# Kernel optimization log

Hardware: AMD Instinct MI355X
Metric: run time of the kernel (lower is better)

The kernel has to match this reference:

```python
import jax, jax.numpy as jnp
import numpy as np


def _scattering(image, mags, phases):
    # image: [B,S,S] real; mags/phases: [J,L,S,S] real (Fourier-domain Morlet filters)
    J = mags.shape[0]
    psi = (mags * jnp.exp(1j * phases)).astype(jnp.complex64)        # [J,L,S,S]
    xf = jnp.fft.fft2(image)                                          # [B,S,S] complex64
    # first-order: modulus of wavelet convolutions, all scales/orientations at once
    u1 = jnp.abs(jnp.fft.ifft2(xf[:, None, None] * psi[None]))        # [B,J,L,S,S]
    s0 = image.mean(axis=(-2, -1))                                    # [B]
    s1 = u1.mean(axis=(2, 3, 4))                                      # [B,J] (orientation-averaged)
    # second-order: only j2 > j1 (the nan-filtered entries in the original)
    s2_parts = []
    for j1 in range(J - 1):  # structural loop over scales, not data dims
        u1f = jnp.fft.fft2(u1[:, j1].astype(jnp.complex64))           # [B,L1,S,S]
        psi2 = psi[j1 + 1:]                                           # [J2,L2,S,S]
        v = jnp.abs(jnp.fft.ifft2(u1f[:, :, None, None] * psi2[None, None]))  # [B,L1,J2,L2,S,S]
        s2_parts.append(v.mean(axis=(1, 3, 4, 5)))                    # [B,J2]
    s2 = jnp.concatenate(s2_parts, axis=1)                            # [B, J*(J-1)/2]
    return s0, s1, s2


def setup_inputs() -> dict:
    key = jax.random.key(0)
    ks = jax.random.split(key, 8)
    B, S, J, L = 64, 128, 6, 4
    return {
        "image_batch": jax.random.normal(ks[0], (B, S, S), dtype=jnp.float32),
        "mags": jax.random.uniform(ks[1], (J, L, S, S), dtype=jnp.float32),
        "phases": jax.random.normal(ks[2], (J, L, S, S), dtype=jnp.float32),
        "w1": jax.random.normal(ks[3], (22, 16), dtype=jnp.float32) * 0.1,
        "b1": jnp.zeros((16,), dtype=jnp.float32),
        "w2": jax.random.normal(ks[4], (16, 16), dtype=jnp.float32) * 0.1,
        "b2": jnp.zeros((16,), dtype=jnp.float32),
        "w3": jax.random.normal(ks[5], (16, 1), dtype=jnp.float32) * 0.1,
        "b3": jnp.zeros((1,), dtype=jnp.float32),
    }


def reference(image_batch, mags, phases, w1, b1, w2, b2, w3, b3):
    s0, s1, s2 = _scattering(image_batch, mags, phases)
    x = jnp.concatenate([s0[:, None], s1, s2], axis=1)                # [B,22]
    x = jax.nn.relu(x @ w1 + b1)
    x = jax.nn.relu(x @ w2 + b2)
    x = jax.nn.sigmoid(x @ w3 + b3)
    return jnp.squeeze(x, axis=1)                                     # [B]
```

## Files before the change

kernel.cpp:

```cpp
#include <hip/hip_runtime.h>
#include <math.h>


#define SDIM 128
#define PLANE 16384
#define PITCH 129
#define NT 1024
#define TWO_PI 6.28318530717958647692f
#define PSIH_SCALE 16.0f
#define A_SCALE 16.0f

typedef _Float16 h2 __attribute__((ext_vector_type(2)));

constexpr float W16R[8] = {1.f, 0.9238795325f, 0.7071067812f, 0.3826834324f,
                           0.f, -0.3826834324f, -0.7071067812f, -0.9238795325f};
constexpr float W16I[8] = {0.f, -0.3826834324f, -0.7071067812f, -0.9238795325f,
                           -1.f, -0.9238795325f, -0.7071067812f, -0.3826834324f};

__device__ __forceinline__ float fast_sqrtf(float x) { return __builtin_amdgcn_sqrtf(x); }

__device__ __forceinline__ unsigned packbf(float re, float im) {
  const unsigned r = __float_as_uint(re) + 0x8000u;
  const unsigned i = __float_as_uint(im) + 0x8000u;
  return __builtin_amdgcn_perm(r, i, 0x07060302u);
}
__device__ __forceinline__ void unpackbf(unsigned u, float& re, float& im) {
  re = __uint_as_float(u & 0xFFFF0000u);
  im = __uint_as_float(u << 16);
}

union UHU { unsigned u; h2 h; };
__device__ __forceinline__ h2 u2h(unsigned u) { UHU x; x.u = u; return x.h; }
__device__ __forceinline__ unsigned h2u(h2 h) { UHU x; x.h = h; return x.u; }
__device__ __forceinline__ h2 bch2(float f) { const _Float16 h = (_Float16)f; h2 v = {h, h}; return v; }
__device__ __forceinline__ h2 mkh2(float a, float b) { h2 v = {(_Float16)a, (_Float16)b}; return v; }

#define SEL_LO 0x05040100u
#define SEL_HI 0x07060302u

__device__ __forceinline__ void stC(float2* s, int idx, float re, float im) { s[idx] = make_float2(re, im); }
__device__ __forceinline__ void ldC(const float2* s, int idx, float& re, float& im) { const float2 v = s[idx]; re = v.x; im = v.y; }
__device__ __forceinline__ void stC(unsigned* s, int idx, float re, float im) { s[idx] = packbf(re, im); }
__device__ __forceinline__ void ldC(const unsigned* s, int idx, float& re, float& im) { unpackbf(s[idx], re, im); }

__device__ __forceinline__ void load_tw(const float2* __restrict__ twg, int g,
                                        float* twr, float* twi) {
#pragma unroll
  for (int k = 1; k < 16; ++k) {
    const float2 w = twg[16 * g + k];
    twr[k] = __uint_as_float(__builtin_amdgcn_readfirstlane(__float_as_uint(w.x)));
    twi[k] = __uint_as_float(__builtin_amdgcn_readfirstlane(__float_as_uint(w.y)));
  }
}
__device__ __forceinline__ void load_twh(const uint2* __restrict__ twgh, int g,
                                         unsigned* twru, unsigned* twiu) {
#pragma unroll
  for (int k = 1; k < 16; ++k) {
    const uint2 w = twgh[16 * g + k];
    twru[k] = (unsigned)__builtin_amdgcn_readfirstlane((int)w.x);
    twiu[k] = (unsigned)__builtin_amdgcn_readfirstlane((int)w.y);
  }
}

template<bool INV>
__device__ __forceinline__ void bfly(float& ar, float& ai, float& br, float& bi, const int idx) {
  float tr, ti;
  if (idx == 0) { tr = br; ti = bi; }
  else if (idx == 4) {
    if (INV) { tr = -bi; ti = br; } else { tr = bi; ti = -br; }
  } else {
    const float wr = W16R[idx];
    const float wi = INV ? -W16I[idx] : W16I[idx];
    tr = br * wr - bi * wi;
    ti = br * wi + bi * wr;
  }
  br = ar - tr; bi = ai - ti;
  ar = ar + tr; ai = ai + ti;
}

#define CSWAP(re, im, a, b) { float _t = re[a]; re[a]=re[b]; re[b]=_t; _t = im[a]; im[a]=im[b]; im[b]=_t; }

template<bool INV>
__device__ __forceinline__ void dft16(float* re, float* im) {
  CSWAP(re, im, 1, 8) CSWAP(re, im, 2, 4) CSWAP(re, im, 3, 12)
  CSWAP(re, im, 5, 10) CSWAP(re, im, 7, 14) CSWAP(re, im, 11, 13)
#pragma unroll
  for (int ls = 1; ls <= 4; ++ls) {
    const int len = 1 << ls, half = len >> 1, tstep = 16 >> ls;
#pragma unroll
    for (int blk = 0; blk < 16; blk += len)
#pragma unroll
      for (int j = 0; j < half; ++j)
        bfly<INV>(re[blk + j], im[blk + j], re[blk + j + half], im[blk + j + half], j * tstep);
  }
}

template<bool INV>
__device__ __forceinline__ void dft8(float* re, float* im) {
  CSWAP(re, im, 1, 4) CSWAP(re, im, 3, 6)
#pragma unroll
  for (int ls = 1; ls <= 3; ++ls) {
    const int len = 1 << ls, half = len >> 1, tstep = 8 >> ls;
#pragma unroll
    for (int blk = 0; blk < 8; blk += len)
#pragma unroll
      for (int j = 0; j < half; ++j)
        bfly<INV>(re[blk + j], im[blk + j], re[blk + j + half], im[blk + j + half], j * tstep * 2);
  }
}

__device__ __forceinline__ void twmul_fwd(float* R, float* I, const float* twr, const float* twi) {
#pragma unroll
  for (int k = 1; k < 16; ++k) {
    const float r = R[k] * twr[k] - I[k] * twi[k];
    I[k] = R[k] * twi[k] + I[k] * twr[k]; R[k] = r;
  }
}
__device__ __forceinline__ void twmul_inv(float* R, float* I, const float* twr, const float* twi) {
#pragma unroll
  for (int k = 1; k < 16; ++k) {
    const float r = R[k] * twr[k] + I[k] * twi[k];
    I[k] = I[k] * twr[k] - R[k] * twi[k]; R[k] = r;
  }
}

template<typename S>
__device__ __forceinline__ void fwd_fft2(float* R, float* I, S* sC,
                                         int g, int q, const float* twr, const float* twi) {
  const int rb = q * PITCH;
  dft16<false>(R, I);
  twmul_fwd(R, I, twr, twi);
  __syncthreads();
#pragma unroll
  for (int k = 0; k < 16; ++k) stC(sC, rb + 8 * k + g, R[k], I[k]);
  __syncthreads();
#pragma unroll
  for (int t = 0; t < 8; ++t) {
    ldC(sC, rb + 16 * g + t, R[t], I[t]);
    ldC(sC, rb + 16 * g + 8 + t, R[8 + t], I[8 + t]);
  }
  dft8<false>(R, I); dft8<false>(R + 8, I + 8);
#pragma unroll
  for (int k2 = 0; k2 < 8; ++k2) {
    stC(sC, rb + 16 * g + k2, R[k2], I[k2]);
    stC(sC, rb + 16 * g + 8 + k2, R[8 + k2], I[8 + k2]);
  }
  __syncthreads();
#pragma unroll
  for (int m = 0; m < 16; ++m) ldC(sC, (g + 8 * m) * PITCH + q, R[m], I[m]);
  dft16<false>(R, I);
  twmul_fwd(R, I, twr, twi);
#pragma unroll
  for (int k = 0; k < 16; ++k) stC(sC, (8 * k + g) * PITCH + q, R[k], I[k]);
  __syncthreads();
#pragma unroll
  for (int u = 0; u < 8; ++u) {
    const int bp = (16 * g + 2 * u) * PITCH + q;
    ldC(sC, bp, R[2 * u], I[2 * u]);
    ldC(sC, bp + PITCH, R[2 * u + 1], I[2 * u + 1]);
  }
  dft8<false>(R, I); dft8<false>(R + 8, I + 8);
}

template<bool FIRST, typename S>
__device__ __forceinline__ void inv_fft2(float* R, float* I, S* sC,
                                         int g, int q, const float* twr, const float* twi) {
  const int rb = q * PITCH;
  dft8<true>(R, I); dft8<true>(R + 8, I + 8);
  if constexpr (!FIRST) __syncthreads();
#pragma unroll
  for (int t = 0; t < 16; ++t) stC(sC, rb + 16 * g + t, R[t], I[t]);
  __syncthreads();
#pragma unroll
  for (int k = 0; k < 16; ++k) ldC(sC, rb + 8 * k + g, R[k], I[k]);
  twmul_inv(R, I, twr, twi);
  dft16<true>(R, I);
#pragma unroll
  for (int m = 0; m < 16; ++m) stC(sC, rb + g + 8 * m, R[m], I[m]);
  __syncthreads();
#pragma unroll
  for (int u = 0; u < 8; ++u) {
    const int bp = (16 * g + 2 * u) * PITCH + q;
    ldC(sC, bp, R[2 * u], I[2 * u]);
    ldC(sC, bp + PITCH, R[2 * u + 1], I[2 * u + 1]);
  }
  dft8<true>(R, I); dft8<true>(R + 8, I + 8);
#pragma unroll
  for (int u = 0; u < 8; ++u) {
    const int bp = (16 * g + 2 * u) * PITCH + q;
    stC(sC, bp, R[2 * u], I[2 * u]);
    stC(sC, bp + PITCH, R[2 * u + 1], I[2 * u + 1]);
  }
  __syncthreads();
#pragma unroll
  for (int k = 0; k < 16; ++k) ldC(sC, (8 * k + g) * PITCH + q, R[k], I[k]);
  twmul_inv(R, I, twr, twi);
  dft16<true>(R, I);
}

template<bool INV>
__device__ __forceinline__ void bfly_h(h2& ar, h2& ai, h2& br, h2& bi, const int idx) {
  h2 tr, ti;
  if (idx == 0) { tr = br; ti = bi; }
  else if (idx == 4) {
    if (INV) { tr = -bi; ti = br; } else { tr = bi; ti = -br; }
  } else {
    const h2 wr = bch2(W16R[idx]);
    const h2 wi = bch2(INV ? -W16I[idx] : W16I[idx]);
    tr = br * wr - bi * wi;
// ... 64 lines not shown
#pragma unroll
  for (int k = 0; k < 16; ++k) { const uint2 v = sU[sb + 8 * k + g]; R2[k] = u2h(v.x); I2[k] = u2h(v.y); }
  twmul_inv_h(R2, I2, twru, twiu);
  dft16h<true>(R2, I2);
#pragma unroll
  for (int m = 0; m < 16; ++m) sU[sb + g + 8 * m] = make_uint2(h2u(R2[m]), h2u(I2[m]));
  __syncthreads();
  {
    const int s_base = (16 * g) & 63;
    const unsigned sel = (g < 4) ? SEL_LO : SEL_HI;
#pragma unroll
    for (int j = 0; j < 16; ++j) {
      const int cb = (s_base + j) * PITCH;
      const uint2 vA = sU[cb + q];
      const uint2 vB = sU[cb + q + 64];
      R2[j] = u2h(__builtin_amdgcn_perm(vB.x, vA.x, sel));
      I2[j] = u2h(__builtin_amdgcn_perm(vB.y, vA.y, sel));
    }
  }
  dft8h<true>(R2, I2); dft8h<true>(R2 + 8, I2 + 8);
  __syncthreads();
#pragma unroll
  for (int s = 0; s < 16; ++s) sU[sb + 16 * g + s] = make_uint2(h2u(R2[s]), h2u(I2[s]));
  __syncthreads();
#pragma unroll
  for (int k = 0; k < 16; ++k) { const uint2 v = sU[sb + 8 * k + g]; R2[k] = u2h(v.x); I2[k] = u2h(v.y); }
  twmul_inv_h(R2, I2, twru, twiu);
  dft16h<true>(R2, I2);
}

__device__ __forceinline__ void fwd_rp_core(h2* R2, h2* I2, uint2* sU,
                                            int g, int q,
                                            const unsigned* twru, const unsigned* twiu) {
  const int sb = q * PITCH;
  dft16h<false>(R2, I2);
  twmul_fwd_h(R2, I2, twru, twiu);
#pragma unroll
  for (int k = 0; k < 16; ++k) sU[sb + 8 * k + g] = make_uint2(h2u(R2[k]), h2u(I2[k]));
  __syncthreads();
#pragma unroll
  for (int t = 0; t < 16; ++t) { const uint2 v = sU[sb + 16 * g + t]; R2[t] = u2h(v.x); I2[t] = u2h(v.y); }
  dft8h<false>(R2, I2); dft8h<false>(R2 + 8, I2 + 8);
#pragma unroll
  for (int t = 0; t < 16; ++t) sU[sb + 16 * g + t] = make_uint2(h2u(R2[t]), h2u(I2[t]));
  __syncthreads();
  {
#pragma unroll
    for (int u = 0; u < 8; ++u) {
      const int cb = (g + 8 * u) * PITCH;
      const uint2 vA = sU[cb + q];
      const uint2 vB = sU[cb + q + 64];
      R2[u]     = u2h(__builtin_amdgcn_perm(vB.x, vA.x, SEL_LO));
      I2[u]     = u2h(__builtin_amdgcn_perm(vB.y, vA.y, SEL_LO));
      R2[u + 8] = u2h(__builtin_amdgcn_perm(vB.x, vA.x, SEL_HI));
      I2[u + 8] = u2h(__builtin_amdgcn_perm(vB.y, vA.y, SEL_HI));
    }
  }
  dft16h<false>(R2, I2);
  twmul_fwd_h(R2, I2, twru, twiu);
  __syncthreads();
#pragma unroll
  for (int k = 0; k < 16; ++k) sU[sb + 8 * k + g] = make_uint2(h2u(R2[k]), h2u(I2[k]));
  __syncthreads();
#pragma unroll
  for (int t = 0; t < 16; ++t) { const uint2 v = sU[sb + 16 * g + t]; R2[t] = u2h(v.x); I2[t] = u2h(v.y); }
  dft8h<false>(R2, I2); dft8h<false>(R2 + 8, I2 + 8);
}

template<int NW>
__device__ __forceinline__ float block_reduce_sum(float v, float* red, int tid) {
#pragma unroll
  for (int o = 32; o > 0; o >>= 1) v += __shfl_down(v, o);
  __syncthreads();
  if ((tid & 63) == 0) red[tid >> 6] = v;
  __syncthreads();
  float t = 0.0f;
  if (tid == 0) {
#pragma unroll
    for (int w = 0; w < NW; ++w) t += red[w];
  }
  return t;
}

__global__ __launch_bounds__(256) void k_psi(const float* __restrict__ mags,
                                             const float* __restrict__ phases,
                                             float2* __restrict__ psi,
                                             float2* __restrict__ twg,
                                             uint2* __restrict__ psih,
                                             uint2* __restrict__ twgh) {
  if (blockIdx.x == 0 && threadIdx.x < 128) {
    const int gg = threadIdx.x >> 4, k = threadIdx.x & 15;
    float sn, cs;
    __sincosf(-TWO_PI * (float)(gg * k) * (1.0f / 128.0f), &sn, &cs);
    twg[threadIdx.x] = make_float2(cs, sn);
    twgh[threadIdx.x] = make_uint2(h2u(bch2(cs)), h2u(bch2(sn)));
  }
  const int gid = blockIdx.x * 256 + threadIdx.x;
  if (gid < 24 * PLANE) {
    const int p = gid >> 14;
    const int rem = gid & (PLANE - 1);
    const int e = rem & 1;
    const int tt = (rem >> 1) & 1023;
    const int i = rem >> 11;
    const int j = 2 * i + e;
    const int g = tt >> 7, q = tt & 127;
    const int pr = 16 * g + j, pc = q;
    const int kr = (pr >> 3) + 16 * (pr & 7);
    const int kc = (pc >> 3) + 16 * (pc & 7);
    const int src = (p << 14) + kr * SDIM + kc;
    const float m = mags[src] * (1.0f / 16384.0f);
    float sn, cs;
    __sincosf(phases[src], &sn, &cs);
    psi[gid] = make_float2(m * cs, m * sn);
  } else if (gid < 24 * PLANE + 20 * 8192) {
    const int c = gid - 24 * PLANE;
    const int pidx = c >> 13;
    const int rem = c & 8191;
    const int j = rem >> 9;
    const int t512 = rem & 511;
    const int g = t512 >> 6, q = t512 & 63;
    const int row = 16 * g + j;
    const int plane = pidx + 4;
    const int kr = (row >> 3) + 16 * (row & 7);
    const int kc0 = (q >> 3) + 16 * (q & 7);
    const int q1 = q + 64;
    const int kc1 = (q1 >> 3) + 16 * (q1 & 7);
    const int src0 = (plane << 14) + kr * SDIM + kc0;
    const int src1 = (plane << 14) + kr * SDIM + kc1;
    const float scl = PSIH_SCALE / 16384.0f;
    const float m0 = mags[src0] * scl;
    const float m1 = mags[src1] * scl;
    float sn0, cs0, sn1, cs1;
    __sincosf(phases[src0], &sn0, &cs0);
    __sincosf(phases[src1], &sn1, &cs1);
    psih[c] = make_uint2(h2u(mkh2(m0 * cs0, m1 * cs1)), h2u(mkh2(m0 * sn0, m1 * sn1)));
  }
}

__global__ __launch_bounds__(NT) void k_img_fft(const float* __restrict__ img,
                                                float2* __restrict__ Xf,
                                                float* __restrict__ s0,
                                                const float2* __restrict__ twg) {
  __shared__ float2 sC[SDIM * PITCH];
  __shared__ float red[16];
  const int tid = threadIdx.x, b = blockIdx.x;
  const int g = __builtin_amdgcn_readfirstlane(tid >> 7);
  const int q = tid & 127;
  float twr[16], twi[16];
  load_tw(twg, g, twr, twi);
  const float* ip = img + b * PLANE;
  float sum = 0.0f;
#pragma unroll
  for (int kk = 0; kk < 16; ++kk) {
    const int e = tid + kk * NT;
    const float v = ip[e];
    sC[(e >> 7) * PITCH + (e & 127)] = make_float2(v, 0.0f);
    sum += v;
  }
  const float tot = block_reduce_sum<16>(sum, red, tid);
  if (tid == 0) s0[b] = tot * (1.0f / 16384.0f);
  __syncthreads();
  float R[16], I[16];
#pragma unroll
  for (int m = 0; m < 16; ++m) { R[m] = sC[q * PITCH + g + 8 * m].x; I[m] = 0.0f; }
  fwd_fft2(R, I, sC, g, q, twr, twi);
  float4* x4 = (float4*)Xf + (size_t)b * 8192 + tid;
#pragma unroll
  for (int i = 0; i < 8; ++i)
    x4[i * 1024] = make_float4(R[2 * i], I[2 * i], R[2 * i + 1], I[2 * i + 1]);
}

__global__ __launch_bounds__(512, 4) void k_scat_ab(const float2* __restrict__ Xf,
                                                    const float2* __restrict__ psi,
                                                    const uint2* __restrict__ psih,
                                                    float* __restrict__ s1num,
                                                    float* __restrict__ s2num,
                                                    const uint2* __restrict__ twgh) {
  __shared__ uint2 sU[64 * PITCH];
  __shared__ float red[8];
  const int tid = threadIdx.x;
  const int g = __builtin_amdgcn_readfirstlane(tid >> 6);
  const int q = tid & 63;
  unsigned twru[16], twiu[16];
  load_twh(twgh, g, twru, twiu);
  const int bid = blockIdx.x;

  int plane, b, sidx, j1 = -1;
  if (bid < 1280) {
    j1 = bid >> 8;
    b = (bid & 255) >> 2;
    const int l1 = bid & 3;
    plane = j1 * 4 + l1;
    sidx = b * 6 + j1;
  } else {
    const int idx = bid - 1280;
    b = idx >> 2;
    plane = 20 + (idx & 3);
    sidx = b * 6 + 5;
  }

  h2 R2[16], I2[16];
  {
    const int t0 = g * 128 + q;
    const float4* xL = (const float4*)Xf + (size_t)b * 8192 + t0;
    const float4* pL = (const float4*)psi + (size_t)plane * 8192 + t0;
#pragma unroll
    for (int i = 0; i < 8; ++i) {
      const float4 xa = xL[i * 1024],      va = pL[i * 1024];
      const float4 xb = xL[i * 1024 + 64], vb = pL[i * 1024 + 64];
      const float reL0 = xa.x * va.x - xa.y * va.y, imL0 = xa.x * va.y + xa.y * va.x;
      const float reH0 = xb.x * vb.x - xb.y * vb.y, imH0 = xb.x * vb.y + xb.y * vb.x;
      const float reL1 = xa.z * va.z - xa.w * va.w, imL1 = xa.z * va.w + xa.w * va.z;
      const float reH1 = xb.z * vb.z - xb.w * vb.w, imH1 = xb.z * vb.w + xb.w * vb.z;
      R2[2 * i]     = mkh2(reL0 * A_SCALE, reH0 * A_SCALE);
      I2[2 * i]     = mkh2(imL0 * A_SCALE, imH0 * A_SCALE);
      R2[2 * i + 1] = mkh2(reL1 * A_SCALE, reH1 * A_SCALE);
      I2[2 * i + 1] = mkh2(imL1 * A_SCALE, imH1 * A_SCALE);
    }
  }
  inv_rp_core(R2, I2, sU, g, q, twru, twiu);

  if (j1 < 0) {
    float s1sum = 0.0f;
#pragma unroll
    for (int m = 0; m < 16; ++m) {
      const h2 sq = R2[m] * R2[m] + I2[m] * I2[m];
      s1sum += fast_sqrtf((float)sq.x) + fast_sqrtf((float)sq.y);
    }
    const float tot = block_reduce_sum<8>(s1sum, red, tid);
    if (tid == 0) atomicAdd(&s1num[sidx], tot);
    return;
  }

  float s1sum = 0.0f;
#pragma unroll
  for (int m = 0; m < 16; ++m) {
    const h2 sq = R2[m] * R2[m] + I2[m] * I2[m];
    const float aL = fast_sqrtf((float)sq.x);
    const float aH = fast_sqrtf((float)sq.y);
    s1sum += aL + aH;
    R2[m] = mkh2(aL * (1.0f / A_SCALE), aH * (1.0f / A_SCALE));
    I2[m] = bch2(0.0f);
  }
  fwd_rp_core(R2, I2, sU, g, q, twru, twiu);

  h2 UR2[16], UI2[16];
#pragma unroll
  for (int j = 0; j < 16; ++j) { UR2[j] = R2[j]; UI2[j] = I2[j]; }
  uint2 buf[16];
  {
    const uint2* ph = psih + (size_t)(4 * j1) * 8192 + tid;
#pragma unroll
    for (int j = 0; j < 16; ++j) buf[j] = ph[j * 512];
  }
  {
    const float tot = block_reduce_sum<8>(s1sum, red, tid);
    if (tid == 0) atomicAdd(&s1num[sidx], tot);
  }

  const int pb = (j1 * (11 - j1)) >> 1;
  const int nit = (5 - j1) * 4;
  float vsum = 0.0f;
  for (int it = 0; it < nit; ++it) {
#pragma unroll
    for (int j = 0; j < 16; ++j) {
      const h2 pr = u2h(buf[j].x), pi = u2h(buf[j].y);
      R2[j] = UR2[j] * pr - UI2[j] * pi;
      I2[j] = UR2[j] * pi + UI2[j] * pr;
    }
    if (it + 1 < nit) {
      const uint2* phn = psih + (size_t)(4 * j1 + it + 1) * 8192 + tid;
#pragma unroll
      for (int j = 0; j < 16; ++j) buf[j] = phn[j * 512];
    }
    __syncthreads();
    inv_rp_core(R2, I2, sU, g, q, twru, twiu);
#pragma unroll
    for (int m = 0; m < 16; ++m) {
      const h2 sq = R2[m] * R2[m] + I2[m] * I2[m];
      vsum += fast_sqrtf((float)sq.x) + fast_sqrtf((float)sq.y);
    }
    if ((it & 3) == 3) {
      const float tot = block_reduce_sum<8>(vsum, red, tid);
      if (tid == 0) atomicAdd(&s2num[b * 15 + pb + (it >> 2)], tot);
      vsum = 0.0f;
    }
  }
}

__global__ __launch_bounds__(NT) void k_scat_a(const float2* __restrict__ Xf,
                                               const float2* __restrict__ psi,
                                               float* __restrict__ s1num,
                                               unsigned* __restrict__ Ubuf,
                                               const float2* __restrict__ twg) {
  __shared__ unsigned sU[SDIM * PITCH];
  __shared__ float red[16];
  const int tid = threadIdx.x;
  const int g = __builtin_amdgcn_readfirstlane(tid >> 7);
  const int q = tid & 127;
  float twr[16], twi[16];
  load_tw(twg, g, twr, twi);
  const int bid = blockIdx.x;
  float R[16], I[16];

  if (bid < 1280) {
    const int j1 = bid >> 8;
    const int b = (bid & 255) >> 2;
    const int l1 = bid & 3;
    const float4* x4 = (const float4*)Xf + (size_t)b * 8192 + tid;
    const float4* p4 = (const float4*)psi + (size_t)(j1 * 4 + l1) * 8192 + tid;
#pragma unroll
    for (int i = 0; i < 8; ++i) {
      const float4 x = x4[i * 1024], v = p4[i * 1024];
      R[2 * i]     = x.x * v.x - x.y * v.y;  I[2 * i]     = x.x * v.y + x.y * v.x;
      R[2 * i + 1] = x.z * v.z - x.w * v.w;  I[2 * i + 1] = x.z * v.w + x.w * v.z;
    }
    inv_fft2<true>(R, I, sU, g, q, twr, twi);
    float s1sum = 0.0f;
#pragma unroll
    for (int m = 0; m < 16; ++m) {
      const float a = fast_sqrtf(R[m] * R[m] + I[m] * I[m]);
      s1sum += a; R[m] = a; I[m] = 0.0f;
    }
    fwd_fft2(R, I, sU, g, q, twr, twi);
    uint4 ob[4];
    unsigned* obs = (unsigned*)ob;
#pragma unroll
    for (int j = 0; j < 16; ++j) obs[j] = packbf(R[j], I[j]);
    uint4* o4 = (uint4*)Ubuf + (size_t)((b * 5 + j1) * 4 + l1) * 4096 + tid;
#pragma unroll
    for (int i = 0; i < 4; ++i) o4[i * 1024] = ob[i];
    const float tot = block_reduce_sum<16>(s1sum, red, tid);
    if (tid == 0) atomicAdd(&s1num[b * 6 + j1], tot);
  } else {
    const int idx = bid - 1280;
    const int b = idx >> 2, l = idx & 3;
    const float4* x4 = (const float4*)Xf + (size_t)b * 8192 + tid;
    const float4* p4 = (const float4*)psi + (size_t)(20 + l) * 8192 + tid;
#pragma unroll
    for (int i = 0; i < 8; ++i) {
      const float4 x = x4[i * 1024], v = p4[i * 1024];
      R[2 * i]     = x.x * v.x - x.y * v.y;  I[2 * i]     = x.x * v.y + x.y * v.x;
      R[2 * i + 1] = x.z * v.z - x.w * v.w;  I[2 * i + 1] = x.z * v.w + x.w * v.z;
    }
    inv_fft2<true>(R, I, sU, g, q, twr, twi);
    float s = 0.0f;
#pragma unroll
    for (int m = 0; m < 16; ++m) s += fast_sqrtf(R[m] * R[m] + I[m] * I[m]);
    const float tot = block_reduce_sum<16>(s, red, tid);
    if (tid == 0) atomicAdd(&s1num[b * 6 + 5], tot);
  }
}

__global__ __launch_bounds__(NT) void k_scat_b(const float2* __restrict__ psi,
                                               const unsigned* __restrict__ Ubuf,
                                               float* __restrict__ s2num,
                                               const float2* __restrict__ twg) {
  __shared__ unsigned sU[SDIM * PITCH];
  __shared__ float red[16];
  const int tid = threadIdx.x;
  const int g = __builtin_amdgcn_readfirstlane(tid >> 7);
  const int q = tid & 127;
  float twr[16], twi[16];
  load_tw(twg, g, twr, twi);
  int t = blockIdx.x;
  const int l2 = t & 3; t >>= 2;
  const int pair = t % 15; t /= 15;
  const int l1 = t & 3;
  const int b = t >> 2;
  int j1 = 0, base = 0;
  if (pair >= 14)      { j1 = 4; base = 14; }
  else if (pair >= 12) { j1 = 3; base = 12; }
  else if (pair >= 9)  { j1 = 2; base = 9; }
  else if (pair >= 5)  { j1 = 1; base = 5; }
  const int j2 = j1 + 1 + (pair - base);
  float R[16], I[16];
  {
    const uint4* u4 = (const uint4*)Ubuf + (size_t)((b * 5 + j1) * 4 + l1) * 4096 + tid;
    uint4 ub[4];
#pragma unroll
    for (int i = 0; i < 4; ++i) ub[i] = u4[i * 1024];
    const unsigned* ubs = (const unsigned*)ub;
    const float4* p4 = (const float4*)psi + (size_t)(j2 * 4 + l2) * 8192 + tid;
#pragma unroll
    for (int i = 0; i < 8; ++i) {
      const float4 v = p4[i * 1024];
      float ur, ui;
      unpackbf(ubs[2 * i], ur, ui);
      R[2 * i] = ur * v.x - ui * v.y;      I[2 * i] = ur * v.y + ui * v.x;
      unpackbf(ubs[2 * i + 1], ur, ui);
      R[2 * i + 1] = ur * v.z - ui * v.w;  I[2 * i + 1] = ur * v.w + ui * v.z;
    }
  }
  inv_fft2<true>(R, I, sU, g, q, twr, twi);
  float vsum = 0.0f;
#pragma unroll
  for (int m = 0; m < 16; ++m) vsum += fast_sqrtf(R[m] * R[m] + I[m] * I[m]);
  const float tot = block_reduce_sum<16>(vsum, red, tid);
  if (tid == 0) atomicAdd(&s2num[b * 15 + pair], tot);
}

__global__ __launch_bounds__(NT) void k_scat_mono(const float2* __restrict__ Xf,
                                                  const float2* __restrict__ psi,
                                                  float* __restrict__ s1num,
                                                  float* __restrict__ s2num,
                                                  const float2* __restrict__ twg) {
  __shared__ unsigned sU[SDIM * PITCH];
  __shared__ float red[16];
  const int tid = threadIdx.x;
  const int g = __builtin_amdgcn_readfirstlane(tid >> 7);
  const int q = tid & 127;
  float twr[16], twi[16];
  load_tw(twg, g, twr, twi);
  const int bid = blockIdx.x;
  float R[16], I[16];
  if (bid < 1280) {
    const int j1 = bid >> 8;
    const int b = (bid & 255) >> 2;
    const int l1 = bid & 3;
    const float4* x4 = (const float4*)Xf + (size_t)b * 8192 + tid;
    const float4* p4 = (const float4*)psi + (size_t)(j1 * 4 + l1) * 8192 + tid;
#pragma unroll
    for (int i = 0; i < 8; ++i) {
      const float4 x = x4[i * 1024], v = p4[i * 1024];
      R[2 * i]     = x.x * v.x - x.y * v.y;  I[2 * i]     = x.x * v.y + x.y * v.x;
      R[2 * i + 1] = x.z * v.z - x.w * v.w;  I[2 * i + 1] = x.z * v.w + x.w * v.z;
    }
    inv_fft2<true>(R, I, sU, g, q, twr, twi);
    float s1sum = 0.0f;
#pragma unroll
    for (int m = 0; m < 16; ++m) {
      const float a = fast_sqrtf(R[m] * R[m] + I[m] * I[m]);
      s1sum += a; R[m] = a; I[m] = 0.0f;
    }
    fwd_fft2(R, I, sU, g, q, twr, twi);
    float Ur[16], Ui[16];
#pragma unroll
    for (int k = 0; k < 16; ++k) { Ur[k] = R[k]; Ui[k] = I[k]; }
    {
      const float tot = block_reduce_sum<16>(s1sum, red, tid);
      if (tid == 0) atomicAdd(&s1num[b * 6 + j1], tot);
    }
    const int pb = (j1 * (11 - j1)) >> 1;
    int plane = (j1 + 1) * 4;
#pragma unroll 1
    for (int j2 = j1 + 1; j2 <= 5; ++j2) {
      float vsum = 0.0f;
#pragma unroll 1
      for (int l2 = 0; l2 < 4; ++l2) {
        const float4* q4 = (const float4*)psi + (size_t)plane * 8192 + tid;
#pragma unroll
        for (int i = 0; i < 8; ++i) {
          const float4 v = q4[i * 1024];
          R[2 * i]     = Ur[2 * i] * v.x - Ui[2 * i] * v.y;
          I[2 * i]     = Ur[2 * i] * v.y + Ui[2 * i] * v.x;
          R[2 * i + 1] = Ur[2 * i + 1] * v.z - Ui[2 * i + 1] * v.w;
          I[2 * i + 1] = Ur[2 * i + 1] * v.w + Ui[2 * i + 1] * v.z;
        }
        inv_fft2<false>(R, I, sU, g, q, twr, twi);
#pragma unroll
        for (int m = 0; m < 16; ++m) vsum += fast_sqrtf(R[m] * R[m] + I[m] * I[m]);
        ++plane;
      }
      const float tot = block_reduce_sum<16>(vsum, red, tid);
      if (tid == 0) atomicAdd(&s2num[b * 15 + pb + (j2 - j1 - 1)], tot);
    }
  } else {
    const int idx = bid - 1280;
    const int b = idx >> 2, l = idx & 3;
    const float4* x4 = (const float4*)Xf + (size_t)b * 8192 + tid;
    const float4* p4 = (const float4*)psi + (size_t)(20 + l) * 8192 + tid;
#pragma unroll
    for (int i = 0; i < 8; ++i) {
      const float4 x = x4[i * 1024], v = p4[i * 1024];
      R[2 * i]     = x.x * v.x - x.y * v.y;  I[2 * i]     = x.x * v.y + x.y * v.x;
      R[2 * i + 1] = x.z * v.z - x.w * v.w;  I[2 * i + 1] = x.z * v.w + x.w * v.z;
    }
    inv_fft2<true>(R, I, sU, g, q, twr, twi);
    float s = 0.0f;
#pragma unroll
    for (int m = 0; m < 16; ++m) s += fast_sqrtf(R[m] * R[m] + I[m] * I[m]);
    const float tot = block_reduce_sum<16>(s, red, tid);
    if (tid == 0) atomicAdd(&s1num[b * 6 + 5], tot);
  }
}

__global__ __launch_bounds__(64) void k_final(const float* __restrict__ s0,
                                              const float* __restrict__ s1num,
                                              const float* __restrict__ s2num,
                                              const float* __restrict__ w1,
                                              const float* __restrict__ b1,
                                              const float* __restrict__ w2,
                                              const float* __restrict__ b2,
                                              const float* __restrict__ w3,
                                              const float* __restrict__ b3,
                                              float* __restrict__ out,
                                              float s1scale, float s2scale) {
  const int b = threadIdx.x;
  if (b >= 64) return;
  float x[22];
  x[0] = s0[b];
#pragma unroll
  for (int j = 0; j < 6; ++j) x[1 + j] = s1num[b * 6 + j] * s1scale;
#pragma unroll
  for (int p = 0; p < 15; ++p) x[7 + p] = s2num[b * 15 + p] * s2scale;
  float h1[16];
#pragma unroll
  for (int o = 0; o < 16; ++o) {
    float t = b1[o];
    for (int i = 0; i < 22; ++i) t += x[i] * w1[i * 16 + o];
    h1[o] = fmaxf(t, 0.0f);
  }
  float h2a[16];
#pragma unroll
  for (int o = 0; o < 16; ++o) {
    float t = b2[o];
    for (int i = 0; i < 16; ++i) t += h1[i] * w2[i * 16 + o];
    h2a[o] = fmaxf(t, 0.0f);
  }
  float t = b3[0];
#pragma unroll
  for (int i = 0; i < 16; ++i) t += h2a[i] * w3[i];
  out[b] = 1.0f / (1.0f + expf(-t));
}

extern "C" void kernel_launch(void* const* d_in, const int* in_sizes, int n_in,
                              void* d_out, int out_size, void* d_ws, size_t ws_size,
                              hipStream_t stream) {
  (void)in_sizes; (void)n_in; (void)out_size;
  const float* image  = (const float*)d_in[0];
  const float* mags   = (const float*)d_in[1];
  const float* phases = (const float*)d_in[2];
  const float* w1 = (const float*)d_in[3];
  const float* b1 = (const float*)d_in[4];
  const float* w2 = (const float*)d_in[5];
  const float* b2 = (const float*)d_in[6];
  const float* w3 = (const float*)d_in[7];
  const float* b3 = (const float*)d_in[8];
  float* out = (float*)d_out;

  char* ws = (char*)d_ws;
  float2* psi = (float2*)ws;
  float2* Xf  = (float2*)(ws + 3145728);
  float*  s0  = (float*)(ws + 11534336);
  float*  s1n = s0 + 64;
  float*  s2n = s1n + 384;
  float2* twg = (float2*)(s2n + 960);
  uint2*  twgh = (uint2*)((char*)twg + 1024);
  unsigned* Ubuf = (unsigned*)(ws + 11542528);
  uint2*  psih = (uint2*)(ws + 95428608);
  const size_t need_r5 = 11542528ull + 83886080ull;
  const size_t need_h2 = need_r5 + 1310720ull;

  hipMemsetAsync(s1n, 0, (384 + 960) * sizeof(float), stream);
  if (ws_size >= need_h2) {
    k_psi<<<dim3(2176), dim3(256), 0, stream>>>(mags, phases, psi, twg, psih, twgh);
    k_img_fft<<<dim3(64), dim3(NT), 0, stream>>>(image, Xf, s0, twg);
    k_scat_ab<<<dim3(1536), dim3(512), 0, stream>>>(Xf, psi, psih, s1n, s2n, twgh);
    k_final<<<dim3(1), dim3(64), 0, stream>>>(s0, s1n, s2n, w1, b1, w2, b2, w3, b3, out,
                                              1.0f / (4.0f * 16384.0f * A_SCALE),
                                              1.0f / (16.0f * 16384.0f * PSIH_SCALE));
  } else if (ws_size >= need_r5) {
    k_psi<<<dim3(1536), dim3(256), 0, stream>>>(mags, phases, psi, twg, psih, twgh);
    k_img_fft<<<dim3(64), dim3(NT), 0, stream>>>(image, Xf, s0, twg);
    k_scat_a<<<dim3(1536), dim3(NT), 0, stream>>>(Xf, psi, s1n, Ubuf, twg);
    k_scat_b<<<dim3(15360), dim3(NT), 0, stream>>>(psi, Ubuf, s2n, twg);
    k_final<<<dim3(1), dim3(64), 0, stream>>>(s0, s1n, s2n, w1, b1, w2, b2, w3, b3, out,
                                              1.0f / (4.0f * 16384.0f),
                                              1.0f / (16.0f * 16384.0f));
  } else {
    k_psi<<<dim3(1536), dim3(256), 0, stream>>>(mags, phases, psi, twg, psih, twgh);
    k_img_fft<<<dim3(64), dim3(NT), 0, stream>>>(image, Xf, s0, twg);
    k_scat_mono<<<dim3(1536), dim3(NT), 0, stream>>>(Xf, psi, s1n, s2n, twg);
    k_final<<<dim3(1), dim3(64), 0, stream>>>(s0, s1n, s2n, w1, b1, w2, b2, w3, b3, out,
                                              1.0f / (4.0f * 16384.0f),
                                              1.0f / (16.0f * 16384.0f));
  }
}
```

Baseline: 424.8 us.

## Merge psi, image FFT and zeroing into one pre-kernel; use fp16 psi everywhere

Filter generation, the image FFT with mean, and the zeroing of the accumulators now run in one `k_pre` launch instead of a memset plus two kernels. The fast path no longer builds an fp32 copy of psi. `k_scat_ab` now forms the first-order product from packed fp16 psih for all 24 planes, which cuts global memory traffic and launch overhead. The fp32 paths that used an intermediate buffer are removed. The cost is that the first-order product is now computed in half precision rather than fp32 with explicit scaling, which may lose accuracy.

Result: faster. 416.0 us (median of 2 runs) (-2.1%).

```diff
diff --git a/kernel.cpp b/kernel.cpp
--- a/kernel.cpp
+++ b/kernel.cpp
@@ -19,16 +19,6 @@
 
 __device__ __forceinline__ float fast_sqrtf(float x) { return __builtin_amdgcn_sqrtf(x); }
 
-__device__ __forceinline__ unsigned packbf(float re, float im) {
-  const unsigned r = __float_as_uint(re) + 0x8000u;
-  const unsigned i = __float_as_uint(im) + 0x8000u;
-  return __builtin_amdgcn_perm(r, i, 0x07060302u);
-}
-__device__ __forceinline__ void unpackbf(unsigned u, float& re, float& im) {
-  re = __uint_as_float(u & 0xFFFF0000u);
-  im = __uint_as_float(u << 16);
-}
-
 union UHU { unsigned u; h2 h; };
 __device__ __forceinline__ h2 u2h(unsigned u) { UHU x; x.u = u; return x.h; }
 __device__ __forceinline__ unsigned h2u(h2 h) { UHU x; x.h = h; return x.u; }
@@ -38,20 +28,6 @@
 #define SEL_LO 0x05040100u
 #define SEL_HI 0x07060302u
 
-__device__ __forceinline__ void stC(float2* s, int idx, float re, float im) { s[idx] = make_float2(re, im); }
-__device__ __forceinline__ void ldC(const float2* s, int idx, float& re, float& im) { const float2 v = s[idx]; re = v.x; im = v.y; }
-__device__ __forceinline__ void stC(unsigned* s, int idx, float re, float im) { s[idx] = packbf(re, im); }
-__device__ __forceinline__ void ldC(const unsigned* s, int idx, float& re, float& im) { unpackbf(s[idx], re, im); }
-
-__device__ __forceinline__ void load_tw(const float2* __restrict__ twg, int g,
-                                        float* twr, float* twi) {
-#pragma unroll
-  for (int k = 1; k < 16; ++k) {
-    const float2 w = twg[16 * g + k];
-    twr[k] = __uint_as_float(__builtin_amdgcn_readfirstlane(__float_as_uint(w.x)));
-    twi[k] = __uint_as_float(__builtin_amdgcn_readfirstlane(__float_as_uint(w.y)));
-  }
-}
 __device__ __forceinline__ void load_twh(const uint2* __restrict__ twgh, int g,
                                          unsigned* twru, unsigned* twiu) {
 #pragma unroll
@@ -125,6 +101,10 @@
 }
 
 template<typename S>
+__device__ __forceinline__ void stC(S* s, int idx, float re, float im) { s[idx] = make_float2(re, im); }
+__device__ __forceinline__ void ldC(const float2* s, int idx, float& re, float& im) { const float2 v = s[idx]; re = v.x; im = v.y; }
+
+template<typename S>
 __device__ __forceinline__ void fwd_fft2(float* R, float* I, S* sC,
                                          int g, int q, const float* twr, const float* twi) {
   const int rb = q * PITCH;
@@ -355,51 +335,42 @@
   return t;
 }
 
-__global__ __launch_bounds__(256) void k_psi(const float* __restrict__ mags,
-                                             const float* __restrict__ phases,
-                                             float2* __restrict__ psi,
-                                             float2* __restrict__ twg,
-                                             uint2* __restrict__ psih,
-                                             uint2* __restrict__ twgh) {
-  if (blockIdx.x == 0 && threadIdx.x < 128) {
-    const int gg = threadIdx.x >> 4, k = threadIdx.x & 15;
-    float sn, cs;
-    __sincosf(-TWO_PI * (float)(gg * k) * (1.0f / 128.0f), &sn, &cs);
-    twg[threadIdx.x] = make_float2(cs, sn);
-    twgh[threadIdx.x] = make_uint2(h2u(bch2(cs)), h2u(bch2(sn)));
-  }
-  const int gid = blockIdx.x * 256 + threadIdx.x;
-  if (gid < 24 * PLANE) {
-    const int p = gid >> 14;
-    const int rem = gid & (PLANE - 1);
-    const int e = rem & 1;
-    const int tt = (rem >> 1) & 1023;
-    const int i = rem >> 11;
-    const int j = 2 * i + e;
-    const int g = tt >> 7, q = tt & 127;
-    const int pr = 16 * g + j, pc = q;
-    const int kr = (pr >> 3) + 16 * (pr & 7);
-    const int kc = (pc >> 3) + 16 * (pc & 7);
-    const int src = (p << 14) + kr * SDIM + kc;
-    const float m = mags[src] * (1.0f / 16384.0f);
-    float sn, cs;
-    __sincosf(phases[src], &sn, &cs);
-    psi[gid] = make_float2(m * cs, m * sn);
-  } else if (gid < 24 * PLANE + 20 * 8192) {
-    const int c = gid - 24 * PLANE;
+__global__ __launch_bounds__(NT) void k_pre(const float* __restrict__ mags,
+                                            const float* __restrict__ phases,
+                                            const float* __restrict__ img,
+                                            uint2* __restrict__ psih,
+                                            uint2* __restrict__ twgh,
+                                            float2* __restrict__ Xf,
+                                            float* __restrict__ s0,
+                                            float* __restrict__ s1n) {
+  __shared__ float2 sC[SDIM * PITCH];
+  __shared__ float2 sTw[128];
+  __shared__ float red[16];
+  const int bid = blockIdx.x, tid = threadIdx.x;
+
+  if (bid < 192) {
+    if (bid == 0) {
+      if (tid < 128) {
+        const int gg = tid >> 4, k = tid & 15;
+        float sn, cs;
+        __sincosf(-TWO_PI * (float)(gg * k) * (1.0f / 128.0f), &sn, &cs);
+        twgh[tid] = make_uint2(h2u(bch2(cs)), h2u(bch2(sn)));
+      }
+      for (int t = tid; t < 1344; t += NT) s1n[t] = 0.0f;
+    }
+    const int c = bid * NT + tid;
     const int pidx = c >> 13;
     const int rem = c & 8191;
     const int j = rem >> 9;
     const int t512 = rem & 511;
     const int g = t512 >> 6, q = t512 & 63;
     const int row = 16 * g + j;
-    const int plane = pidx + 4;
     const int kr = (row >> 3) + 16 * (row & 7);
     const int kc0 = (q >> 3) + 16 * (q & 7);
     const int q1 = q + 64;
     const int kc1 = (q1 >> 3) + 16 * (q1 & 7);
-    const int src0 = (plane << 14) + kr * SDIM + kc0;
-    const int src1 = (plane << 14) + kr * SDIM + kc1;
+    const int src0 = (pidx << 14) + kr * SDIM + kc0;
+    const int src1 = (pidx << 14) + kr * SDIM + kc1;
     const float scl = PSIH_SCALE / 16384.0f;
     const float m0 = mags[src0] * scl;
     const float m1 = mags[src1] * scl;
@@ -407,6 +378,201 @@
     __sincosf(phases[src0], &sn0, &cs0);
     __sincosf(phases[src1], &sn1, &cs1);
     psih[c] = make_uint2(h2u(mkh2(m0 * cs0, m1 * cs1)), h2u(mkh2(m0 * sn0, m1 * sn1)));
+    return;
+  }
+
+  const int b = bid - 192;
+  const int g = __builtin_amdgcn_readfirstlane(tid >> 7);
+  const int q = tid & 127;
+  if (tid < 128) {
+    const int gg = tid >> 4, k = tid & 15;
+    float sn, cs;
+    __sincosf(-TWO_PI * (float)(gg * k) * (1.0f / 128.0f), &sn, &cs);
+    sTw[tid] = make_float2(cs, sn);
+  }
+  const float* ip = img + b * PLANE;
+  float sum = 0.0f;
+#pragma unroll
+  for (int kk = 0; kk < 16; ++kk) {
+    const int e = tid + kk * NT;
+    const float v = ip[e];
+    sC[(e >> 7) * PITCH + (e & 127)] = make_float2(v, 0.0f);
+    sum += v;
+  }
+  const float tot = block_reduce_sum<16>(sum, red, tid);
+  if (tid == 0) s0[b] = tot * (1.0f / 16384.0f);
+  __syncthreads();
+  float twr[16], twi[16];
+#pragma unroll
+  for (int k = 1; k < 16; ++k) {
+    const float2 w = sTw[16 * g + k];
+    twr[k] = __uint_as_float(__builtin_amdgcn_readfirstlane(__float_as_uint(w.x)));
+    twi[k] = __uint_as_float(__builtin_amdgcn_readfirstlane(__float_as_uint(w.y)));
+  }
+  float R[16], I[16];
+#pragma unroll
+  for (int m = 0; m < 16; ++m) { R[m] = sC[q * PITCH + g + 8 * m].x; I[m] = 0.0f; }
+  fwd_fft2(R, I, sC, g, q, twr, twi);
+  float4* x4 = (float4*)Xf + (size_t)b * 8192 + tid;
+#pragma unroll
+  for (int i = 0; i < 8; ++i)
+    x4[i * 1024] = make_float4(R[2 * i], I[2 * i], R[2 * i + 1], I[2 * i + 1]);
+}
+
+__global__ __launch_bounds__(512, 4) void k_scat_ab(const float2* __restrict__ Xf,
+                                                    const uint2* __restrict__ psih,
+                                                    float* __restrict__ s1num,
+                                                    float* __restrict__ s2num,
+                                                    const uint2* __restrict__ twgh) {
+  __shared__ uint2 sU[64 * PITCH];
+  __shared__ float red[8];
+  const int tid = threadIdx.x;
+  const int g = __builtin_amdgcn_readfirstlane(tid >> 6);
+  const int q = tid & 63;
+  unsigned twru[16], twiu[16];
+  load_twh(twgh, g, twru, twiu);
+  const int bid = blockIdx.x;
+
+  int plane, b, sidx, j1 = -1;
+  if (bid < 1280) {
+    j1 = bid >> 8;
+    b = (bid & 255) >> 2;
+    const int l1 = bid & 3;
+    plane = j1 * 4 + l1;
+    sidx = b * 6 + j1;
+  } else {
+    const int idx = bid - 1280;
+    b = idx >> 2;
+    plane = 20 + (idx & 3);
+    sidx = b * 6 + 5;
+  }
+
+  h2 R2[16], I2[16];
+  {
+    const int t0 = g * 128 + q;
+    const float4* xL = (const float4*)Xf + (size_t)b * 8192 + t0;
+    const uint2* ph = psih + (size_t)plane * 8192 + tid;
+#pragma unroll
+    for (int i = 0; i < 8; ++i) {
+      const float4 xa = xL[i * 1024];
+      const float4 xb = xL[i * 1024 + 64];
+      const h2 XR0 = mkh2(xa.x, xb.x), XI0 = mkh2(xa.y, xb.y);
+      const h2 XR1 = mkh2(xa.z, xb.z), XI1 = mkh2(xa.w, xb.w);
+      const uint2 p0 = ph[(2 * i) * 512];
+      const uint2 p1 = ph[(2 * i + 1) * 512];
+      const h2 PR0 = u2h(p0.x), PI0 = u2h(p0.y);
+      const h2 PR1 = u2h(p1.x), PI1 = u2h(p1.y);
+      R2[2 * i]     = XR0 * PR0 - XI0 * PI0;
+      I2[2 * i]     = XR0 * PI0 + XI0 * PR0;
+      R2[2 * i + 1] = XR1 * PR1 - XI1 * PI1;
+      I2[2 * i + 1] = XR1 * PI1 + XI1 * PR1;
+    }
+  }
+  inv_rp_core(R2, I2, sU, g, q, twru, twiu);
+
+  if (j1 < 0) {
+    float s1sum = 0.0f;
+#pragma unroll
+    for (int m = 0; m < 16; ++m) {
+      const h2 sq = R2[m] * R2[m] + I2[m] * I2[m];
+      s1sum += fast_sqrtf((float)sq.x) + fast_sqrtf((float)sq.y);
+    }
+    const float tot = block_reduce_sum<8>(s1sum, red, tid);
+    if (tid == 0) atomicAdd(&s1num[sidx], tot);
+    return;
+  }
+
+  float s1sum = 0.0f;
+#pragma unroll
+  for (int m = 0; m < 16; ++m) {
+    const h2 sq = R2[m] * R2[m] + I2[m] * I2[m];
+    const float aL = fast_sqrtf((float)sq.x);
+    const float aH = fast_sqrtf((float)sq.y);
+    s1sum += aL + aH;
+    R2[m] = mkh2(aL * (1.0f / A_SCALE), aH * (1.0f / A_SCALE));
+    I2[m] = bch2(0.0f);
+  }
+  fwd_rp_core(R2, I2, sU, g, q, twru, twiu);
+
+  h2 UR2[16], UI2[16];
+#pragma unroll
+  for (int j = 0; j < 16; ++j) { UR2[j] = R2[j]; UI2[j] = I2[j]; }
+  uint2 buf[16];
+  {
+    const uint2* ph = psih + (size_t)(4 * j1 + 4) * 8192 + tid;
+#pragma unroll
+    for (int j = 0; j < 16; ++j) buf[j] = ph[j * 512];
+  }
+  {
+    const float tot = block_reduce_sum<8>(s1sum, red, tid);
+    if (tid == 0) atomicAdd(&s1num[sidx], tot);
+  }
+
+  const int pb = (j1 * (11 - j1)) >> 1;
+  const int nit = (5 - j1) * 4;
+  float vsum = 0.0f;
+  for (int it = 0; it < nit; ++it) {
+#pragma unroll
+    for (int j = 0; j < 16; ++j) {
+      const h2 pr = u2h(buf[j].x), pi = u2h(buf[j].y);
+      R2[j] = UR2[j] * pr - UI2[j] * pi;
+      I2[j] = UR2[j] * pi + UI2[j] * pr;
+    }
+    if (it + 1 < nit) {
+      const uint2* phn = psih + (size_t)(4 * j1 + 4 + it + 1) * 8192 + tid;
+#pragma unroll
+      for (int j = 0; j < 16; ++j) buf[j] = phn[j * 512];
+    }
+    __syncthreads();
+    inv_rp_core(R2, I2, sU, g, q, twru, twiu);
+#pragma unroll
+    for (int m = 0; m < 16; ++m) {
+      const h2 sq = R2[m] * R2[m] + I2[m] * I2[m];
+      vsum += fast_sqrtf((float)sq.x) + fast_sqrtf((float)sq.y);
+    }
+    if ((it & 3) == 3) {
+      const float tot = block_reduce_sum<8>(vsum, red, tid);
+      if (tid == 0) atomicAdd(&s2num[b * 15 + pb + (it >> 2)], tot);
+      vsum = 0.0f;
+    }
+  }
+}
+
+__global__ __launch_bounds__(256) void k_psi_f32(const float* __restrict__ mags,
+                                                 const float* __restrict__ phases,
+                                                 float2* __restrict__ psi,
+                                                 float2* __restrict__ twg) {
+  if (blockIdx.x == 0 && threadIdx.x < 128) {
+    const int gg = threadIdx.x >> 4, k = threadIdx.x & 15;
+    float sn, cs;
+    __sincosf(-TWO_PI * (float)(gg * k) * (1.0f / 128.0f), &sn, &cs);
+    twg[threadIdx.x] = make_float2(cs, sn);
+  }
+  const int gid = blockIdx.x * 256 + threadIdx.x;
+  const int p = gid >> 14;
+  const int rem = gid & (PLANE - 1);
+  const int e = rem & 1;
+  const int tt = (rem >> 1) & 1023;
+  const int i = rem >> 11;
+  const int j = 2 * i + e;
+  const int g = tt >> 7, q = tt & 127;
+  const int pr = 16 * g + j, pc = q;
+  const int kr = (pr >> 3) + 16 * (pr & 7);
+  const int kc = (pc >> 3) + 16 * (pc & 7);
+  const int src = (p << 14) + kr * SDIM + kc;
+  const float m = mags[src] * (1.0f / 16384.0f);
+  float sn, cs;
+  __sincosf(phases[src], &sn, &cs);
+  psi[gid] = make_float2(m * cs, m * sn);
+}
+
+__device__ __forceinline__ void load_tw(const float2* __restrict__ twg, int g,
+                                        float* twr, float* twi) {
+#pragma unroll
+  for (int k = 1; k < 16; ++k) {
+    const float2 w = twg[16 * g + k];
+    twr[k] = __uint_as_float(__builtin_amdgcn_readfirstlane(__float_as_uint(w.x)));
+    twi[k] = __uint_as_float(__builtin_amdgcn_readfirstlane(__float_as_uint(w.y)));
   }
 }
 
@@ -443,242 +609,12 @@
     x4[i * 1024] = make_float4(R[2 * i], I[2 * i], R[2 * i + 1], I[2 * i + 1]);
 }
 
-__global__ __launch_bounds__(512, 4) void k_scat_ab(const float2* __restrict__ Xf,
-                                                    const float2* __restrict__ psi,
-                                                    const uint2* __restrict__ psih,
-                                                    float* __restrict__ s1num,
-                                                    float* __restrict__ s2num,
-                                                    const uint2* __restrict__ twgh) {
-  __shared__ uint2 sU[64 * PITCH];
-  __shared__ float red[8];
-  const int tid = threadIdx.x;
-  const int g = __builtin_amdgcn_readfirstlane(tid >> 6);
-  const int q = tid & 63;
-  unsigned twru[16], twiu[16];
-  load_twh(twgh, g, twru, twiu);
-  const int bid = blockIdx.x;
-
-  int plane, b, sidx, j1 = -1;
-  if (bid < 1280) {
-    j1 = bid >> 8;
-    b = (bid & 255) >> 2;
-    const int l1 = bid & 3;
-    plane = j1 * 4 + l1;
-    sidx = b * 6 + j1;
-  } else {
-    const int idx = bid - 1280;
-    b = idx >> 2;
-    plane = 20 + (idx & 3);
-    sidx = b * 6 + 5;
-  }
-
-  h2 R2[16], I2[16];
-  {
-    const int t0 = g * 128 + q;
-    const float4* xL = (const float4*)Xf + (size_t)b * 8192 + t0;
-    const float4* pL = (const float4*)psi + (size_t)plane * 8192 + t0;
-#pragma unroll
-    for (int i = 0; i < 8; ++i) {
-      const float4 xa = xL[i * 1024],      va = pL[i * 1024];
-      const float4 xb = xL[i * 1024 + 64], vb = pL[i * 1024 + 64];
-      const float reL0 = xa.x * va.x - xa.y * va.y, imL0 = xa.x * va.y + xa.y * va.x;
-      const float reH0 = xb.x * vb.x - xb.y * vb.y, imH0 = xb.x * vb.y + xb.y * vb.x;
-      const float reL1 = xa.z * va.z - xa.w * va.w, imL1 = xa.z * va.w + xa.w * va.z;
-      const float reH1 = xb.z * vb.z - xb.w * vb.w, imH1 = xb.z * vb.w + xb.w * vb.z;
-      R2[2 * i]     = mkh2(reL0 * A_SCALE, reH0 * A_SCALE);
-      I2[2 * i]     = mkh2(imL0 * A_SCALE, imH0 * A_SCALE);
-      R2[2 * i + 1] = mkh2(reL1 * A_SCALE, reH1 * A_SCALE);
-      I2[2 * i + 1] = mkh2(imL1 * A_SCALE, imH1 * A_SCALE);
-    }
-  }
-  inv_rp_core(R2, I2, sU, g, q, twru, twiu);
-
-  if (j1 < 0) {
-    float s1sum = 0.0f;
-#pragma unroll
-    for (int m = 0; m < 16; ++m) {
-      const h2 sq = R2[m] * R2[m] + I2[m] * I2[m];
-      s1sum += fast_sqrtf((float)sq.x) + fast_sqrtf((float)sq.y);
-    }
-    const float tot = block_reduce_sum<8>(s1sum, red, tid);
-    if (tid == 0) atomicAdd(&s1num[sidx], tot);
-    return;
-  }
-
-  float s1sum = 0.0f;
-#pragma unroll
-  for (int m = 0; m < 16; ++m) {
-    const h2 sq = R2[m] * R2[m] + I2[m] * I2[m];
-    const float aL = fast_sqrtf((float)sq.x);
-    const float aH = fast_sqrtf((float)sq.y);
-    s1sum += aL + aH;
-    R2[m] = mkh2(aL * (1.0f / A_SCALE), aH * (1.0f / A_SCALE));
-    I2[m] = bch2(0.0f);
-  }
-  fwd_rp_core(R2, I2, sU, g, q, twru, twiu);
-
-  h2 UR2[16], UI2[16];
-#pragma unroll
-  for (int j = 0; j < 16; ++j) { UR2[j] = R2[j]; UI2[j] = I2[j]; }
-  uint2 buf[16];
-  {
-    const uint2* ph = psih + (size_t)(4 * j1) * 8192 + tid;
-#pragma unroll
-    for (int j = 0; j < 16; ++j) buf[j] = ph[j * 512];
-  }
-  {
-    const float tot = block_reduce_sum<8>(s1sum, red, tid);
-    if (tid == 0) atomicAdd(&s1num[sidx], tot);
-  }
-
-  const int pb = (j1 * (11 - j1)) >> 1;
-  const int nit = (5 - j1) * 4;
-  float vsum = 0.0f;
-  for (int it = 0; it < nit; ++it) {
-#pragma unroll
-    for (int j = 0; j < 16; ++j) {
-      const h2 pr = u2h(buf[j].x), pi = u2h(buf[j].y);
-      R2[j] = UR2[j] * pr - UI2[j] * pi;
-      I2[j] = UR2[j] * pi + UI2[j] * pr;
-    }
-    if (it + 1 < nit) {
-      const uint2* phn = psih + (size_t)(4 * j1 + it + 1) * 8192 + tid;
-#pragma unroll
-      for (int j = 0; j < 16; ++j) buf[j] = phn[j * 512];
-    }
-    __syncthreads();
-    inv_rp_core(R2, I2, sU, g, q, twru, twiu);
-#pragma unroll
-    for (int m = 0; m < 16; ++m) {
-      const h2 sq = R2[m] * R2[m] + I2[m] * I2[m];
-      vsum += fast_sqrtf((float)sq.x) + fast_sqrtf((float)sq.y);
-    }
-    if ((it & 3) == 3) {
-      const float tot = block_reduce_sum<8>(vsum, red, tid);
-      if (tid == 0) atomicAdd(&s2num[b * 15 + pb + (it >> 2)], tot);
-      vsum = 0.0f;
-    }
-  }
-}
-
-__global__ __launch_bounds__(NT) void k_scat_a(const float2* __restrict__ Xf,
-                                               const float2* __restrict__ psi,
-                                               float* __restrict__ s1num,
-                                               unsigned* __restrict__ Ubuf,
-                                               const float2* __restrict__ twg) {
-  __shared__ unsigned sU[SDIM * PITCH];
-  __shared__ float red[16];
-  const int tid = threadIdx.x;
-  const int g = __builtin_amdgcn_readfirstlane(tid >> 7);
-  const int q = tid & 127;
-  float twr[16], twi[16];
-  load_tw(twg, g, twr, twi);
-  const int bid = blockIdx.x;
-  float R[16], I[16];
-
-  if (bid < 1280) {
-    const int j1 = bid >> 8;
-    const int b = (bid & 255) >> 2;
-    const int l1 = bid & 3;
-    const float4* x4 = (const float4*)Xf + (size_t)b * 8192 + tid;
-    const float4* p4 = (const float4*)psi + (size_t)(j1 * 4 + l1) * 8192 + tid;
-#pragma unroll
-    for (int i = 0; i < 8; ++i) {
-      const float4 x = x4[i * 1024], v = p4[i * 1024];
-      R[2 * i]     = x.x * v.x - x.y * v.y;  I[2 * i]     = x.x * v.y + x.y * v.x;
-      R[2 * i + 1] = x.z * v.z - x.w * v.w;  I[2 * i + 1] = x.z * v.w + x.w * v.z;
-    }
-    inv_fft2<true>(R, I, sU, g, q, twr, twi);
-    float s1sum = 0.0f;
-#pragma unroll
-    for (int m = 0; m < 16; ++m) {
-      const float a = fast_sqrtf(R[m] * R[m] + I[m] * I[m]);
-      s1sum += a; R[m] = a; I[m] = 0.0f;
-    }
-    fwd_fft2(R, I, sU, g, q, twr, twi);
-    uint4 ob[4];
-    unsigned* obs = (unsigned*)ob;
-#pragma unroll
-    for (int j = 0; j < 16; ++j) obs[j] = packbf(R[j], I[j]);
-    uint4* o4 = (uint4*)Ubuf + (size_t)((b * 5 + j1) * 4 + l1) * 4096 + tid;
-#pragma unroll
-    for (int i = 0; i < 4; ++i) o4[i * 1024] = ob[i];
-    const float tot = block_reduce_sum<16>(s1sum, red, tid);
-    if (tid == 0) atomicAdd(&s1num[b * 6 + j1], tot);
-  } else {
-    const int idx = bid - 1280;
-    const int b = idx >> 2, l = idx & 3;
-    const float4* x4 = (const float4*)Xf + (size_t)b * 8192 + tid;
-    const float4* p4 = (const float4*)psi + (size_t)(20 + l) * 8192 + tid;
-#pragma unroll
-    for (int i = 0; i < 8; ++i) {
-      const float4 x = x4[i * 1024], v = p4[i * 1024];
-      R[2 * i]     = x.x * v.x - x.y * v.y;  I[2 * i]     = x.x * v.y + x.y * v.x;
-      R[2 * i + 1] = x.z * v.z - x.w * v.w;  I[2 * i + 1] = x.z * v.w + x.w * v.z;
-    }
-    inv_fft2<true>(R, I, sU, g, q, twr, twi);
-    float s = 0.0f;
-#pragma unroll
-    for (int m = 0; m < 16; ++m) s += fast_sqrtf(R[m] * R[m] + I[m] * I[m]);
-    const float tot = block_reduce_sum<16>(s, red, tid);
-    if (tid == 0) atomicAdd(&s1num[b * 6 + 5], tot);
-  }
-}
-
-__global__ __launch_bounds__(NT) void k_scat_b(const float2* __restrict__ psi,
-                                               const unsigned* __restrict__ Ubuf,
-                                               float* __restrict__ s2num,
-                                               const float2* __restrict__ twg) {
-  __shared__ unsigned sU[SDIM * PITCH];
-  __shared__ float red[16];
-  const int tid = threadIdx.x;
-  const int g = __builtin_amdgcn_readfirstlane(tid >> 7);
-  const int q = tid & 127;
-  float twr[16], twi[16];
-  load_tw(twg, g, twr, twi);
-  int t = blockIdx.x;
-  const int l2 = t & 3; t >>= 2;
-  const int pair = t % 15; t /= 15;
-  const int l1 = t & 3;
-  const int b = t >> 2;
-  int j1 = 0, base = 0;
-  if (pair >= 14)      { j1 = 4; base = 14; }
-  else if (pair >= 12) { j1 = 3; base = 12; }
-  else if (pair >= 9)  { j1 = 2; base = 9; }
-  else if (pair >= 5)  { j1 = 1; base = 5; }
-  const int j2 = j1 + 1 + (pair - base);
-  float R[16], I[16];
-  {
-    const uint4* u4 = (const uint4*)Ubuf + (size_t)((b * 5 + j1) * 4 + l1) * 4096 + tid;
-    uint4 ub[4];
-#pragma unroll
-    for (int i = 0; i < 4; ++i) ub[i] = u4[i * 1024];
-    const unsigned* ubs = (const unsigned*)ub;
-    const float4* p4 = (const float4*)psi + (size_t)(j2 * 4 + l2) * 8192 + tid;
-#pragma unroll
-    for (int i = 0; i < 8; ++i) {
-      const float4 v = p4[i * 1024];
-      float ur, ui;
-      unpackbf(ubs[2 * i], ur, ui);
-      R[2 * i] = ur * v.x - ui * v.y;      I[2 * i] = ur * v.y + ui * v.x;
-      unpackbf(ubs[2 * i + 1], ur, ui);
-      R[2 * i + 1] = ur * v.z - ui * v.w;  I[2 * i + 1] = ur * v.w + ui * v.z;
-    }
-  }
-  inv_fft2<true>(R, I, sU, g, q, twr, twi);
-  float vsum = 0.0f;
-#pragma unroll
-  for (int m = 0; m < 16; ++m) vsum += fast_sqrtf(R[m] * R[m] + I[m] * I[m]);
-  const float tot = block_reduce_sum<16>(vsum, red, tid);
-  if (tid == 0) atomicAdd(&s2num[b * 15 + pair], tot);
-}
-
 __global__ __launch_bounds__(NT) void k_scat_mono(const float2* __restrict__ Xf,
                                                   const float2* __restrict__ psi,
                                                   float* __restrict__ s1num,
                                                   float* __restrict__ s2num,
                                                   const float2* __restrict__ twg) {
-  __shared__ unsigned sU[SDIM * PITCH];
+  __shared__ float2 sU[SDIM * PITCH];
   __shared__ float red[16];
   const int tid = threadIdx.x;
   const int g = __builtin_amdgcn_readfirstlane(tid >> 7);
@@ -813,36 +749,26 @@
   float* out = (float*)d_out;
 
   char* ws = (char*)d_ws;
-  float2* psi = (float2*)ws;
+  uint2*  psih = (uint2*)ws;
+  float2* psi  = (float2*)ws;
   float2* Xf  = (float2*)(ws + 3145728);
   float*  s0  = (float*)(ws + 11534336);
   float*  s1n = s0 + 64;
   float*  s2n = s1n + 384;
   float2* twg = (float2*)(s2n + 960);
   uint2*  twgh = (uint2*)((char*)twg + 1024);
-  unsigned* Ubuf = (unsigned*)(ws + 11542528);
-  uint2*  psih = (uint2*)(ws + 95428608);
-  const size_t need_r5 = 11542528ull + 83886080ull;
-  const size_t need_h2 = need_r5 + 1310720ull;
-
-  hipMemsetAsync(s1n, 0, (384 + 960) * sizeof(float), stream);
+  const size_t need_h2 = 11534336ull + (64 + 1344) * 4 + 2048;
+
   if (ws_size >= need_h2) {
-    k_psi<<<dim3(2176), dim3(256), 0, stream>>>(mags, phases, psi, twg, psih, twgh);
-    k_img_fft<<<dim3(64), dim3(NT), 0, stream>>>(image, Xf, s0, twg);
-    k_scat_ab<<<dim3(1536), dim3(512), 0, stream>>>(Xf, psi, psih, s1n, s2n, twgh);
+    k_pre<<<dim3(256), dim3(NT), 0, stream>>>(mags, phases, image, psih, twgh,
+                                              Xf, s0, s1n);
+    k_scat_ab<<<dim3(1536), dim3(512), 0, stream>>>(Xf, psih, s1n, s2n, twgh);
     k_final<<<dim3(1), dim3(64), 0, stream>>>(s0, s1n, s2n, w1, b1, w2, b2, w3, b3, out,
                                               1.0f / (4.0f * 16384.0f * A_SCALE),
                                               1.0f / (16.0f * 16384.0f * PSIH_SCALE));
-  } else if (ws_size >= need_r5) {
-    k_psi<<<dim3(1536), dim3(256), 0, stream>>>(mags, phases, psi, twg, psih, twgh);
-    k_img_fft<<<dim3(64), dim3(NT), 0, stream>>>(image, Xf, s0, twg);
-    k_scat_a<<<dim3(1536), dim3(NT), 0, stream>>>(Xf, psi, s1n, Ubuf, twg);
-    k_scat_b<<<dim3(15360), dim3(NT), 0, stream>>>(psi, Ubuf, s2n, twg);
-    k_final<<<dim3(1), dim3(64), 0, stream>>>(s0, s1n, s2n, w1, b1, w2, b2, w3, b3, out,
-                                              1.0f / (4.0f * 16384.0f),
-                                              1.0f / (16.0f * 16384.0f));
   } else {
-    k_psi<<<dim3(1536), dim3(256), 0, stream>>>(mags, phases, psi, twg, psih, twgh);
+    hipMemsetAsync(s1n, 0, (384 + 960) * sizeof(float), stream);
+    k_psi_f32<<<dim3(1536), dim3(256), 0, stream>>>(mags, phases, psi, twg);
     k_img_fft<<<dim3(64), dim3(NT), 0, stream>>>(image, Xf, s0, twg);
     k_scat_mono<<<dim3(1536), dim3(NT), 0, stream>>>(Xf, psi, s1n, s2n, twg);
     k_final<<<dim3(1), dim3(64), 0, stream>>>(s0, s1n, s2n, w1, b1, w2, b2, w3, b3, out,
```
